# Optimization experiments

Hardware: AMD Instinct MI355X
Metric: run time of the kernel (lower is better)

## Reference

```python
import jax, jax.numpy as jnp
import numpy as np

T, B, OBS, H, P, L, A = 512, 128, 512, 256, 128, 4, 4


def _ln(x, scale, bias, eps=1e-6):
    mu = jnp.mean(x, axis=-1, keepdims=True)
    var = jnp.mean((x - mu) ** 2, axis=-1, keepdims=True)
    return (x - mu) * jax.lax.rsqrt(var + eps) * scale + bias


def _binop(qi, qj):
    # S5 reset-aware associative operator: elements (A, b, reset_flag)
    Ai, bi, ci = qi
    Aj, bj, cj = qj
    A = (Aj * Ai) * (1.0 - cj) + Aj * cj
    b = (Aj * bi + bj) * (1.0 - cj) + bj * cj
    c = ci * (1.0 - cj) + cj
    return A, b, c


def _s5_layer(x, dones, h0, scale, bias, lam_re, lam_im, b_re, b_im, c_re, c_im, d_vec, log_step, glu_W, glu_b):
    # x: (T,B,H) real, dones: (T,B), h0: (B,P) complex64
    skip = x
    u = _ln(x, scale, bias)                                  # prenorm
    lam = lam_re + 1j * lam_im                               # (P,)
    step = jnp.exp(log_step)                                 # (P,)
    lam_bar = jnp.exp(lam * step)                            # ZOH discretization
    B_bar = ((lam_bar - 1.0) / lam)[:, None] * (b_re + 1j * b_im)  # (P,H)
    Bu = jnp.einsum('tbh,ph->tbp', u.astype(jnp.complex64), B_bar)  # (T,B,P)
    A_el = jnp.concatenate([jnp.ones((1, B, P), jnp.complex64),
                            jnp.broadcast_to(lam_bar.astype(jnp.complex64), (T, B, P))], axis=0)
    b_el = jnp.concatenate([h0[None], Bu], axis=0)
    c_el = jnp.concatenate([jnp.zeros((1, B, 1), jnp.float32), dones[..., None]], axis=0)
    _, xs, _ = jax.lax.associative_scan(_binop, (A_el, b_el, c_el), axis=0)
    xs = xs[1:]                                              # (T,B,P) complex states
    new_h = xs[-1]
    C = c_re + 1j * c_im                                     # (H,P)
    ys = 2.0 * jnp.real(jnp.einsum('tbp,hp->tbh', xs, C)) + d_vec * u  # conj_sym output + D*u
    z = _ln(ys, scale, bias)                                 # gtrxl norm (shared LayerNorm params)
    z = jax.nn.gelu(z)                                       # half_glu1
    z = z * jax.nn.sigmoid(z @ glu_W + glu_b)
    return skip + z, new_h


def setup_inputs() -> dict:
    key = jax.random.key(0)
    ks = jax.random.split(key, 40)
    f32 = jnp.float32

    def n(i, shape, s=1.0):
        return jax.random.normal(ks[i], shape, f32) * s

    inp = {}
    inp['obs'] = n(0, (T, B, OBS))
    inp['dones'] = (jax.random.uniform(ks[1], (T, B)) < 0.01).astype(f32)
    inp['hidden_re'] = jnp.zeros((L, B, P), f32)
    inp['hidden_im'] = jnp.zeros((L, B, P), f32)
    inp['enc0_W'] = n(2, (OBS, 128), 1.0 / np.sqrt(OBS))
    inp['enc0_b'] = jnp.zeros((128,), f32)
    inp['enc1_W'] = n(3, (128, H), 1.0 / np.sqrt(128))
    inp['enc1_b'] = jnp.zeros((H,), f32)
    inp['norm_scale'] = jnp.ones((L, H), f32)
    inp['norm_bias'] = jnp.zeros((L, H), f32)
    inp['Lambda_re'] = -0.5 * jax.random.uniform(ks[4], (L, P), f32) - 0.1
    inp['Lambda_im'] = n(5, (L, P), np.pi)
    inp['B_re'] = n(6, (L, P, H), 1.0 / np.sqrt(H))
    inp['B_im'] = n(7, (L, P, H), 1.0 / np.sqrt(H))
    inp['C_re'] = n(8, (L, H, P), 1.0 / np.sqrt(2 * P))
    inp['C_im'] = n(9, (L, H, P), 1.0 / np.sqrt(2 * P))
    inp['D'] = n(10, (L, H))
    inp['log_step'] = jax.random.uniform(ks[11], (L, P), f32, np.log(1e-3), np.log(1e-1))
    inp['glu_W'] = n(12, (L, H, H), 1.0 / np.sqrt(H))
    inp['glu_b'] = jnp.zeros((L, H), f32)
    inp['ab0_W'] = n(13, (H, 128), 1.0 / np.sqrt(H))
    inp['ab0_b'] = jnp.zeros((128,), f32)
    inp['ab1_W'] = n(14, (128, 128), 1.0 / np.sqrt(128))
    inp['ab1_b'] = jnp.zeros((128,), f32)
    inp['adec_W'] = n(15, (128, A), 0.01 / np.sqrt(128))
    inp['adec_b'] = jnp.full((A,), 0.5, f32)
    inp['log_std'] = jnp.full((A,), -0.7, f32)
    inp['vb0_W'] = n(16, (H, 128), 1.0 / np.sqrt(H))
    inp['vb0_b'] = jnp.zeros((128,), f32)
    inp['vb1_W'] = n(17, (128, 128), 1.0 / np.sqrt(128))
    inp['vb1_b'] = jnp.zeros((128,), f32)
    inp['vdec_W'] = n(18, (128, 1), 1.0 / np.sqrt(128))
    inp['vdec_b'] = jnp.zeros((1,), f32)
    return inp


def reference(obs, dones, hidden_re, hidden_im, enc0_W, enc0_b, enc1_W, enc1_b,
              norm_scale, norm_bias, Lambda_re, Lambda_im, B_re, B_im, C_re, C_im,
              D, log_step, glu_W, glu_b, ab0_W, ab0_b, ab1_W, ab1_b, adec_W, adec_b,
              log_std, vb0_W, vb0_b, vb1_W, vb1_b, vdec_W, vdec_b):
    e = jax.nn.leaky_relu(obs @ enc0_W + enc0_b)
    e = jax.nn.leaky_relu(e @ enc1_W + enc1_b)
    h0 = (hidden_re + 1j * hidden_im).astype(jnp.complex64)  # (L,B,P)
    new_h = []
    for l in range(L):
        e, hl = _s5_layer(e, dones, h0[l], norm_scale[l], norm_bias[l],
                          Lambda_re[l], Lambda_im[l], B_re[l], B_im[l],
                          C_re[l], C_im[l], D[l], log_step[l], glu_W[l], glu_b[l])
        new_h.append(hl)
    new_h = jnp.stack(new_h)
    am = jax.nn.leaky_relu(e @ ab0_W + ab0_b)
    am = jax.nn.leaky_relu(am @ ab1_W + ab1_b)
    am = am @ adec_W + adec_b                                # actor mean (T,B,A)
    v = jax.nn.leaky_relu(e @ vb0_W + vb0_b)
    v = jax.nn.leaky_relu(v @ vb1_W + vb1_b)
    v = v @ vdec_W + vdec_b                                  # critic (T,B,1)
    sc = jnp.broadcast_to(jnp.exp(log_std), am.shape)        # Normal scale (pi params)
    out = jnp.concatenate([am, sc, v], axis=-1)              # (T,B,2A+1)
    return out, jnp.real(new_h), jnp.imag(new_h)
```

## Files before the change

kernel.cpp:

```cpp
#include <hip/hip_runtime.h>
#include <math.h>

#define TT 512
#define BB 128
#define OBSD 512
#define HD 256
#define PD 128
#define LD 4
#define NTB (TT*BB)

typedef __bf16 bf16x8 __attribute__((ext_vector_type(8)));
typedef float  f32x4  __attribute__((ext_vector_type(4)));

__device__ __forceinline__ float bf2f(unsigned short u) {
    return __uint_as_float(((unsigned)u) << 16);
}
__device__ __forceinline__ unsigned short f2bf(float f) {
    unsigned u = __float_as_uint(f);
    unsigned r = (u + 0x7FFFu + ((u >> 16) & 1u)) >> 16;
    return (unsigned short)r;
}
__device__ __forceinline__ float gelu_f(float x) {
    float x3 = x * x * x;
    return 0.5f * x * (1.f + tanhf(0.7978845608028654f * (x + 0.044715f * x3)));
}

template<int MODE, int NJ>
__global__ __launch_bounds__(256) void mgemm2(
    const unsigned short* __restrict__ A, const unsigned short* __restrict__ BT,
    int K, const float* __restrict__ bias,
    const float* __restrict__ lnsc, const float* __restrict__ lnbi,
    const unsigned short* __restrict__ aux1, unsigned short* Xio,
    unsigned short* __restrict__ U, int wU)
{
    const int N = NJ * 64;
    __shared__ unsigned short smA[64 * 32];
    __shared__ unsigned short smB[NJ * 64 * 32];
    __shared__ float2 red[64][4];
    int tid = threadIdx.x;
    int lane = tid & 63, w = tid >> 6;
    int m16 = lane & 15, quad = lane >> 4;
    int m0 = blockIdx.x * 64;

    f32x4 acc[4][NJ] = {};

    for (int k0 = 0; k0 < K; k0 += 32) {
        {
            const unsigned short* g = A + (size_t)(m0 + (tid >> 2)) * K + k0 + (tid & 3) * 8;
            unsigned short* l = smA + tid * 8;
            __builtin_amdgcn_global_load_lds(
                (const __attribute__((address_space(1))) void*)g,
                (__attribute__((address_space(3))) void*)l, 16, 0, 0);
        }
#pragma unroll
        for (int p = 0; p < NJ; ++p) {
            const unsigned short* g = BT + (size_t)(p * 64 + (tid >> 2)) * K + k0 + (tid & 3) * 8;
            unsigned short* l = smB + p * 2048 + tid * 8;
            __builtin_amdgcn_global_load_lds(
                (const __attribute__((address_space(1))) void*)g,
                (__attribute__((address_space(3))) void*)l, 16, 0, 0);
        }
        __syncthreads();
        bf16x8 af[4], bfr[NJ];
#pragma unroll
        for (int mi = 0; mi < 4; ++mi)
            af[mi] = *(const bf16x8*)(smA + (mi * 16 + m16) * 32 + quad * 8);
#pragma unroll
        for (int nj = 0; nj < NJ; ++nj)
            bfr[nj] = *(const bf16x8*)(smB + (w * NJ * 16 + nj * 16 + m16) * 32 + quad * 8);
#pragma unroll
        for (int mi = 0; mi < 4; ++mi)
#pragma unroll
            for (int nj = 0; nj < NJ; ++nj)
                acc[mi][nj] = __builtin_amdgcn_mfma_f32_16x16x32_bf16(
                    bfr[nj], af[mi], acc[mi][nj], 0, 0, 0);
        __syncthreads();
    }

    int colb = w * NJ * 16 + quad * 4;

    if (MODE == 1) {
#pragma unroll
        for (int mi = 0; mi < 4; ++mi) {
            size_t rowb = (size_t)(m0 + mi * 16 + m16) * N;
#pragma unroll
            for (int nj = 0; nj < NJ; ++nj) {
                ushort4 o = { f2bf(acc[mi][nj][0]), f2bf(acc[mi][nj][1]),
                              f2bf(acc[mi][nj][2]), f2bf(acc[mi][nj][3]) };
                *(ushort4*)(U + rowb + colb + nj * 16) = o;
            }
        }
        return;
    }

    float4 bn[NJ];
#pragma unroll
    for (int nj = 0; nj < NJ; ++nj) bn[nj] = *(const float4*)(bias + colb + nj * 16);

#pragma unroll
    for (int mi = 0; mi < 4; ++mi) {
        size_t rowb = (size_t)(m0 + mi * 16 + m16) * N;
        float s = 0.f, q = 0.f;
#pragma unroll
        for (int nj = 0; nj < NJ; ++nj) {
            ushort4 a1, xo;
            if (MODE == 2 || MODE == 3) a1 = *(const ushort4*)(aux1 + rowb + colb + nj * 16);
            if (MODE == 3)              xo = *(const ushort4*)(Xio + rowb + colb + nj * 16);
            float vv[4];
#pragma unroll
            for (int r = 0; r < 4; ++r) {
                float v = acc[mi][nj][r];
                float bv = (r == 0) ? bn[nj].x : (r == 1) ? bn[nj].y : (r == 2) ? bn[nj].z : bn[nj].w;
                if (MODE == 0 || MODE == 4) {
                    v += bv; v = v > 0.f ? v : 0.01f * v;
                } else if (MODE == 2) {
                    float u = bf2f(r == 0 ? a1.x : r == 1 ? a1.y : r == 2 ? a1.z : a1.w);
                    v += bv * u;
                } else if (MODE == 3) {
                    float zz = bf2f(r == 0 ? a1.x : r == 1 ? a1.y : r == 2 ? a1.z : a1.w);
                    float xx = bf2f(r == 0 ? xo.x : r == 1 ? xo.y : r == 2 ? xo.z : xo.w);
                    float sg = 1.f / (1.f + expf(-(v + bv)));
                    v = xx + zz * sg;
                }
                vv[r] = v;
                acc[mi][nj][r] = v;
                s += v; q += v * v;
            }
            if (MODE == 0 || MODE == 3) {
                ushort4 o = { f2bf(vv[0]), f2bf(vv[1]), f2bf(vv[2]), f2bf(vv[3]) };
                *(ushort4*)(Xio + rowb + colb + nj * 16) = o;
            } else if (MODE == 4) {
                ushort4 o = { f2bf(vv[0]), f2bf(vv[1]), f2bf(vv[2]), f2bf(vv[3]) };
                *(ushort4*)(U + rowb + colb + nj * 16) = o;
            }
        }
        if (MODE != 4 && (MODE != 3 || wU)) {
            s += __shfl_xor(s, 16); q += __shfl_xor(q, 16);
            s += __shfl_xor(s, 32); q += __shfl_xor(q, 32);
            if (quad == 0) red[mi * 16 + m16][w] = float2{s, q};
        }
    }
    if (MODE == 4 || (MODE == 3 && !wU)) return;
    __syncthreads();

    float4 ls[NJ], lb[NJ];
#pragma unroll
    for (int nj = 0; nj < NJ; ++nj) {
        ls[nj] = *(const float4*)(lnsc + colb + nj * 16);
        lb[nj] = *(const float4*)(lnbi + colb + nj * 16);
    }
#pragma unroll
    for (int mi = 0; mi < 4; ++mi) {
        int row_l = mi * 16 + m16;
        float2 t0 = red[row_l][0], t1 = red[row_l][1], t2 = red[row_l][2], t3 = red[row_l][3];
        float S = t0.x + t1.x + t2.x + t3.x;
        float Q = t0.y + t1.y + t2.y + t3.y;
        float mu = S * (1.f / 256.f);
        float var = Q * (1.f / 256.f) - mu * mu;
        float rstd = rsqrtf(var + 1e-6f);
        size_t rowb = (size_t)(m0 + row_l) * N;
#pragma unroll
        for (int nj = 0; nj < NJ; ++nj) {
            float o[4];
#pragma unroll
            for (int r = 0; r < 4; ++r) {
                float sc = (r == 0) ? ls[nj].x : (r == 1) ? ls[nj].y : (r == 2) ? ls[nj].z : ls[nj].w;
                float bi = (r == 0) ? lb[nj].x : (r == 1) ? lb[nj].y : (r == 2) ? lb[nj].z : lb[nj].w;
                float v = (acc[mi][nj][r] - mu) * rstd * sc + bi;
                if (MODE == 2) v = gelu_f(v);
                o[r] = v;
            }
            ushort4 ov = { f2bf(o[0]), f2bf(o[1]), f2bf(o[2]), f2bf(o[3]) };
            *(ushort4*)(U + rowb + colb + nj * 16) = ov;
        }
    }
}

__global__ __launch_bounds__(256) void mgemm_obs(
    const float* __restrict__ A, const unsigned short* __restrict__ BT,
    unsigned short* __restrict__ U, const float* __restrict__ bias)
{
    const int K = 512, NJ = 2, N = 128;
    __shared__ unsigned short smA[64 * 32];
    __shared__ unsigned short smB[NJ * 64 * 32];
    int tid = threadIdx.x;
    int lane = tid & 63, w = tid >> 6;
    int m16 = lane & 15, quad = lane >> 4;
    int m0 = blockIdx.x * 64;

    f32x4 acc[4][NJ] = {};
    for (int k0 = 0; k0 < K; k0 += 32) {
#pragma unroll
        for (int p = 0; p < 2; ++p) {
            int idx = p * 256 + tid;
            int r = idx >> 3, kq = (idx & 7) * 4;
            float4 v = *(const float4*)(A + (size_t)(m0 + r) * K + k0 + kq);
            ushort4 o = { f2bf(v.x), f2bf(v.y), f2bf(v.z), f2bf(v.w) };
            *(ushort4*)(smA + r * 32 + kq) = o;
        }
#pragma unroll
        for (int p = 0; p < NJ; ++p) {
            const unsigned short* g = BT + (size_t)(p * 64 + (tid >> 2)) * K + k0 + (tid & 3) * 8;
            unsigned short* l = smB + p * 2048 + tid * 8;
            __builtin_amdgcn_global_load_lds(
                (const __attribute__((address_space(1))) void*)g,
                (__attribute__((address_space(3))) void*)l, 16, 0, 0);
        }
        __syncthreads();
        bf16x8 af[4], bfr[NJ];
#pragma unroll
        for (int mi = 0; mi < 4; ++mi)
            af[mi] = *(const bf16x8*)(smA + (mi * 16 + m16) * 32 + quad * 8);
#pragma unroll
        for (int nj = 0; nj < NJ; ++nj)
            bfr[nj] = *(const bf16x8*)(smB + (w * NJ * 16 + nj * 16 + m16) * 32 + quad * 8);
#pragma unroll
        for (int mi = 0; mi < 4; ++mi)
#pragma unroll
            for (int nj = 0; nj < NJ; ++nj)
                acc[mi][nj] = __builtin_amdgcn_mfma_f32_16x16x32_bf16(
                    bfr[nj], af[mi], acc[mi][nj], 0, 0, 0);
        __syncthreads();
    }
    int colb = w * NJ * 16 + quad * 4;
#pragma unroll
    for (int mi = 0; mi < 4; ++mi) {
        size_t rowb = (size_t)(m0 + mi * 16 + m16) * N;
#pragma unroll
        for (int nj = 0; nj < NJ; ++nj) {
            float4 bv = *(const float4*)(bias + colb + nj * 16);
            float v0 = acc[mi][nj][0] + bv.x; v0 = v0 > 0.f ? v0 : 0.01f * v0;
            float v1 = acc[mi][nj][1] + bv.y; v1 = v1 > 0.f ? v1 : 0.01f * v1;
            float v2 = acc[mi][nj][2] + bv.z; v2 = v2 > 0.f ? v2 : 0.01f * v2;
            float v3 = acc[mi][nj][3] + bv.w; v3 = v3 > 0.f ? v3 : 0.01f * v3;
            ushort4 o = { f2bf(v0), f2bf(v1), f2bf(v2), f2bf(v3) };
            *(ushort4*)(U + rowb + colb + nj * 16) = o;
        }
    }
}

__global__ __launch_bounds__(512) void scan2_k(
    const unsigned short* __restrict__ bu, unsigned short* __restrict__ xs,
    const float* __restrict__ dones,
    const float* __restrict__ h0re, const float* __restrict__ h0im,
    const float* __restrict__ lamre, const float* __restrict__ lamim,
    const float* __restrict__ lstep,
    float* __restrict__ outre, float* __restrict__ outim)
{
    __shared__ float sdone[TT];
    __shared__ float4 ssum[8][64];
    __shared__ float2 shin[8][64];
    int tid = threadIdx.x;
    int b  = blockIdx.x >> 1;
    int ph = blockIdx.x & 1;
    int chunk = tid >> 6, pl = tid & 63;
    int p = ph * 64 + pl;
    sdone[tid] = dones[tid * BB + b];
    float lr = lamre[p], li = lamim[p];
    float st = expf(lstep[p]);
    float er = expf(lr * st);
    float ar = er * cosf(li * st);
    float ai = er * sinf(li * st);
    __syncthreads();

    int t0 = chunk * 64;
    unsigned buf[64];
    float Ar = 1.f, Ai = 0.f, br = 0.f, bi = 0.f;
#pragma unroll
    for (int j = 0; j < 64; ++j) {
        size_t off = ((size_t)(t0 + j) * BB + b) * 256 + 2 * p;
        unsigned v = *(const unsigned*)(bu + off);
        buf[j] = v;
        float bur = bf2f((unsigned short)(v & 0xFFFFu));
        float bui = bf2f((unsigned short)(v >> 16));
        if (sdone[t0 + j] != 0.f) {
            Ar = 0.f; Ai = 0.f; br = bur; bi = bui;
        } else {
            float nAr = ar * Ar - ai * Ai;
            float nAi = ar * Ai + ai * Ar;
            float nbr = fmaf(ar, br, fmaf(-ai, bi, bur));
            float nbi = fmaf(ar, bi, fmaf(ai, br, bui));
            Ar = nAr; Ai = nAi; br = nbr; bi = nbi;
        }
    }
    ssum[chunk][pl] = float4{Ar, Ai, br, bi};
    __syncthreads();
    if (tid < 64) {
        int gid = b * 128 + p;
        float hr = h0re[gid], hi = h0im[gid];
#pragma unroll
        for (int c = 0; c < 8; ++c) {
            shin[c][pl] = float2{hr, hi};
            float4 s = ssum[c][pl];
            float nhr = fmaf(s.x, hr, fmaf(-s.y, hi, s.z));
            float nhi = fmaf(s.x, hi, fmaf(s.y, hr, s.w));
            hr = nhr; hi = nhi;
        }
        outre[gid] = hr; outim[gid] = hi;
    }
    __syncthreads();
    float hr = shin[chunk][pl].x, hi = shin[chunk][pl].y;
#pragma unroll
    for (int j = 0; j < 64; ++j) {
        unsigned v = buf[j];
        float bur = bf2f((unsigned short)(v & 0xFFFFu));
        float bui = bf2f((unsigned short)(v >> 16));
        float nr, ni;
        if (sdone[t0 + j] != 0.f) { nr = bur; ni = bui; }
        else {
            nr = fmaf(ar, hr, fmaf(-ai, hi, bur));
            ni = fmaf(ar, hi, fmaf(ai, hr, bui));
        }
        hr = nr; hi = ni;
        size_t off = ((size_t)(t0 + j) * BB + b) * 256 + 2 * p;
        *(unsigned*)(xs + off) = ((unsigned)f2bf(ni) << 16) | f2bf(nr);
    }
}

__global__ __launch_bounds__(256) void prep_k(
    const float* __restrict__ Br, const float* __restrict__ Bi,
    const float* __restrict__ Cr, const float* __restrict__ Ci,
    const float* __restrict__ Lr, const float* __restrict__ Li,
    const float* __restrict__ ls, unsigned short* bbarT, unsigned short* ccatT)
{
    int gid = blockIdx.x * 256 + threadIdx.x;
    int l = gid >> 15;
    int rem = gid & 32767;
    int p = rem >> 8;
    int h = rem & 255;
    float lr = Lr[l * PD + p], li = Li[l * PD + p];
    float st = expf(ls[l * PD + p]);
    float er = expf(lr * st);
    float lbr = er * cosf(li * st);
    float lbi = er * sinf(li * st);
    float nr = lbr - 1.f, ni = lbi;
    float den = lr * lr + li * li;
    float fr = (nr * lr + ni * li) / den;
    float fi = (ni * lr - nr * li) / den;
    float bre = Br[(size_t)(l * PD + p) * HD + h];
    float bim = Bi[(size_t)(l * PD + p) * HD + h];
    size_t lb = (size_t)l * 65536;
    bbarT[lb + (size_t)(2 * p) * 256 + h]     = f2bf(fr * bre - fi * bim);
    bbarT[lb + (size_t)(2 * p + 1) * 256 + h] = f2bf(fr * bim + fi * bre);
    float cre = Cr[(size_t)(l * HD + h) * PD + p];
    float cim = Ci[(size_t)(l * HD + h) * PD + p];
    ccatT[lb + (size_t)h * 256 + 2 * p]     = f2bf(2.f * cre);
    ccatT[lb + (size_t)h * 256 + 2 * p + 1] = f2bf(-2.f * cim);
}

__global__ __launch_bounds__(256) void tcvt_k(const float* __restrict__ in,
    unsigned short* __restrict__ out, int K, int N)
{
    int gid = blockIdx.x * 256 + threadIdx.x;
    if (gid >= K * N) return;
    int k = gid / N, n = gid - k * N;
    out[(size_t)n * K + k] = f2bf(in[gid]);
}

__global__ __launch_bounds__(256) void head_k(
    const unsigned short* __restrict__ am2, const unsigned short* __restrict__ v2,
    const float* __restrict__ adW, const float* __restrict__ adb,
    const float* __restrict__ lstd,
    const float* __restrict__ vdW, const float* __restrict__ vdb,
    float* out)
{
    int wid = threadIdx.x >> 6, lane = threadIdx.x & 63;
    size_t row = (size_t)blockIdx.x * 4 + wid;
    float a1 = bf2f(am2[row * 128 + lane]);
    float a2 = bf2f(am2[row * 128 + 64 + lane]);
    float w1 = bf2f(v2[row * 128 + lane]);
    float w2 = bf2f(v2[row * 128 + 64 + lane]);
    float vals[5];
#pragma unroll
    for (int a = 0; a < 4; ++a)
        vals[a] = a1 * adW[lane * 4 + a] + a2 * adW[(lane + 64) * 4 + a];
    vals[4] = w1 * vdW[lane] + w2 * vdW[64 + lane];
#pragma unroll
    for (int off = 32; off; off >>= 1)
#pragma unroll
        for (int k = 0; k < 5; ++k) vals[k] += __shfl_xor(vals[k], off);
    if (lane == 0) {
        size_t o = row * 9;
#pragma unroll
        for (int a = 0; a < 4; ++a) out[o + a] = vals[a] + adb[a];
#pragma unroll
        for (int a = 0; a < 4; ++a) out[o + 4 + a] = expf(lstd[a]);
        out[o + 8] = vals[4] + vdb[0];
    }
}

extern "C" void kernel_launch(void* const* d_in, const int* in_sizes, int n_in,
                              void* d_out, int out_size, void* d_ws, size_t ws_size,
                              hipStream_t stream) {
    (void)in_sizes; (void)n_in; (void)out_size; (void)ws_size;
    const float* obs     = (const float*)d_in[0];
    const float* dones   = (const float*)d_in[1];
    const float* hre     = (const float*)d_in[2];
    const float* him     = (const float*)d_in[3];
    const float* enc0_W  = (const float*)d_in[4];
    const float* enc0_b  = (const float*)d_in[5];
    const float* enc1_W  = (const float*)d_in[6];
    const float* enc1_b  = (const float*)d_in[7];
    const float* nsc     = (const float*)d_in[8];
    const float* nbi     = (const float*)d_in[9];
    const float* Lre     = (const float*)d_in[10];
    const float* Lim     = (const float*)d_in[11];
    const float* B_re    = (const float*)d_in[12];
    const float* B_im    = (const float*)d_in[13];
    const float* C_re    = (const float*)d_in[14];
    const float* C_im    = (const float*)d_in[15];
    const float* Dv      = (const float*)d_in[16];
    const float* lstep   = (const float*)d_in[17];
    const float* glu_W   = (const float*)d_in[18];
    const float* glu_b   = (const float*)d_in[19];
    const float* ab0_W   = (const float*)d_in[20];
    const float* ab0_b   = (const float*)d_in[21];
    const float* ab1_W   = (const float*)d_in[22];
    const float* ab1_b   = (const float*)d_in[23];
    const float* adec_W  = (const float*)d_in[24];
    const float* adec_b  = (const float*)d_in[25];
    const float* log_std = (const float*)d_in[26];
    const float* vb0_W   = (const float*)d_in[27];
    const float* vb0_b   = (const float*)d_in[28];
    const float* vb1_W   = (const float*)d_in[29];
    const float* vb1_b   = (const float*)d_in[30];
    const float* vdec_W  = (const float*)d_in[31];
    const float* vdec_b  = (const float*)d_in[32];

    const size_t MB = (size_t)1 << 20;
    char* wsb = (char*)d_ws;
    unsigned short* XS    = (unsigned short*)(wsb);
    unsigned short* AM1   = (unsigned short*)(wsb);
    unsigned short* V1    = (unsigned short*)(wsb + 16 * MB);
    unsigned short* AM2   = (unsigned short*)(wsb + 32 * MB);
    unsigned short* V2    = (unsigned short*)(wsb + 48 * MB);
    unsigned short* U1    = (unsigned short*)(wsb + 64 * MB);
    unsigned short* X     = (unsigned short*)(wsb + 96 * MB);
    unsigned short* U     = (unsigned short*)(wsb + 128 * MB);
    unsigned short* BU    = (unsigned short*)(wsb + 160 * MB);
    char* wgt = wsb + 192 * MB;
    unsigned short* BBART = (unsigned short*)(wgt);
    unsigned short* CCATT = (unsigned short*)(wgt + 512 * 1024);
    unsigned short* GLUT  = (unsigned short*)(wgt + 1024 * 1024);
    unsigned short* E0T   = (unsigned short*)(wgt + 1536 * 1024);
    unsigned short* E1T   = (unsigned short*)(wgt + 1664 * 1024);
    unsigned short* AB0T  = (unsigned short*)(wgt + 1728 * 1024);
    unsigned short* AB1T  = (unsigned short*)(wgt + 1792 * 1024);
    unsigned short* VB0T  = (unsigned short*)(wgt + 1824 * 1024);
    unsigned short* VB1T  = (unsigned short*)(wgt + 1888 * 1024);

    float* out   = (float*)d_out;
    float* outre = out + (size_t)NTB * 9;
    float* outim = outre + LD * BB * PD;

    prep_k<<<512, 256, 0, stream>>>(B_re, B_im, C_re, C_im, Lre, Lim, lstep, BBART, CCATT);
    tcvt_k<<<256, 256, 0, stream>>>(enc0_W, E0T, 512, 128);
    tcvt_k<<<128, 256, 0, stream>>>(enc1_W, E1T, 128, 256);
    for (int l = 0; l < LD; ++l)
        tcvt_k<<<256, 256, 0, stream>>>(glu_W + (size_t)l * 65536, GLUT + (size_t)l * 65536, 256, 256);
    tcvt_k<<<128, 256, 0, stream>>>(ab0_W, AB0T, 256, 128);
    tcvt_k<<<64, 256, 0, stream>>>(ab1_W, AB1T, 128, 128);
    tcvt_k<<<128, 256, 0, stream>>>(vb0_W, VB0T, 256, 128);
    tcvt_k<<<64, 256, 0, stream>>>(vb1_W, VB1T, 128, 128);

    mgemm_obs<<<1024, 256, 0, stream>>>(obs, E0T, U1, enc0_b);
    mgemm2<0, 4><<<1024, 256, 0, stream>>>(U1, E1T, 128, enc1_b, nsc, nbi, nullptr, X, U, 1);

    for (int l = 0; l < LD; ++l) {
        mgemm2<1, 4><<<1024, 256, 0, stream>>>(U, BBART + (size_t)l * 65536, 256,
                                               nullptr, nullptr, nullptr, nullptr, nullptr, BU, 0);
        scan2_k<<<256, 512, 0, stream>>>(BU, XS, dones, hre + l * BB * PD, him + l * BB * PD,
                                         Lre + l * PD, Lim + l * PD, lstep + l * PD,
                                         outre + l * BB * PD, outim + l * BB * PD);
        mgemm2<2, 4><<<1024, 256, 0, stream>>>(XS, CCATT + (size_t)l * 65536, 256,
                                               Dv + l * HD, nsc + l * HD, nbi + l * HD, U, nullptr, U, 1);
        const float* nsc2 = nsc + ((l + 1 < LD) ? (l + 1) * HD : 0);
        const float* nbi2 = nbi + ((l + 1 < LD) ? (l + 1) * HD : 0);
        mgemm2<3, 4><<<1024, 256, 0, stream>>>(U, GLUT + (size_t)l * 65536, 256,
                                               glu_b + l * HD, nsc2, nbi2, U, X, U, (l + 1 < LD) ? 1 : 0);
    }

    mgemm2<4, 2><<<1024, 256, 0, stream>>>(X, AB0T, 256, ab0_b, nullptr, nullptr, nullptr, nullptr, AM1, 0);
    mgemm2<4, 2><<<1024, 256, 0, stream>>>(AM1, AB1T, 128, ab1_b, nullptr, nullptr, nullptr, nullptr, AM2, 0);
    mgemm2<4, 2><<<1024, 256, 0, stream>>>(X, VB0T, 256, vb0_b, nullptr, nullptr, nullptr, nullptr, V1, 0);
    mgemm2<4, 2><<<1024, 256, 0, stream>>>(V1, VB1T, 128, vb1_b, nullptr, nullptr, nullptr, nullptr, V2, 0);
    head_k<<<NTB / 4, 256, 0, stream>>>(AM2, V2, adec_W, adec_b, log_std, vdec_W, vdec_b, out);
}
```

Baseline: 984.7 us.

## Fuse chained per-layer GEMMs through LDS-resident intermediates and merge head MLPs

Replaces the separate C-projection, GLU and next-layer B-projection GEMM launches with one fused kernel per layer. Each block keeps its 64-row normalized activation tile in shared memory and feeds it straight into the next GEMM. This avoids writing and re-reading the U intermediate through global memory and cuts the number of launches. The actor and critic head MLPs plus the decoder are fused into a single two-way grid kernel, and the weight transposes are merged into one launch. The cost is much larger shared-memory use per block (about 34KB for the z buffer plus a larger B tile), which may lower occupancy.

```diff
diff --git a/kernel.cpp b/kernel.cpp
--- a/kernel.cpp
+++ b/kernel.cpp
@@ -24,130 +24,115 @@
     float x3 = x * x * x;
     return 0.5f * x * (1.f + tanhf(0.7978845608028654f * (x + 0.044715f * x3)));
 }
-
-template<int MODE, int NJ>
-__global__ __launch_bounds__(256) void mgemm2(
-    const unsigned short* __restrict__ A, const unsigned short* __restrict__ BT,
-    int K, const float* __restrict__ bias,
-    const float* __restrict__ lnsc, const float* __restrict__ lnbi,
-    const unsigned short* __restrict__ aux1, unsigned short* Xio,
-    unsigned short* __restrict__ U, int wU)
-{
-    const int N = NJ * 64;
+__device__ __forceinline__ float lane4(float4 v, int r) {
+    return (r == 0) ? v.x : (r == 1) ? v.y : (r == 2) ? v.z : v.w;
+}
+
+__device__ __forceinline__ void stgA(const unsigned short* A, int ldk, int m0, int k0,
+                                     unsigned short* smA, int tid)
+{
+    const unsigned short* g = A + (size_t)(m0 + (tid >> 2)) * ldk + k0 + (tid & 3) * 8;
+    __builtin_amdgcn_global_load_lds(
+        (const __attribute__((address_space(1))) void*)g,
+        (__attribute__((address_space(3))) void*)(smA + tid * 8), 16, 0, 0);
+}
+template<int NR>
+__device__ __forceinline__ void stgB(const unsigned short* BT, int ldk, int k0,
+                                     unsigned short* smB, int tid)
+{
+#pragma unroll
+    for (int p = 0; p < NR / 64; ++p) {
+        const unsigned short* g = BT + (size_t)(p * 64 + (tid >> 2)) * ldk + k0 + (tid & 3) * 8;
+        __builtin_amdgcn_global_load_lds(
+            (const __attribute__((address_space(1))) void*)g,
+            (__attribute__((address_space(3))) void*)(smB + p * 2048 + tid * 8), 16, 0, 0);
+    }
+}
+
+template<int VAR>
+__global__ __launch_bounds__(256, 2) void fused_k(
+    const unsigned short* __restrict__ A, const unsigned short* __restrict__ BT1, int K1,
+    const float* __restrict__ bias1, const float* __restrict__ ln1s, const float* __restrict__ ln1b,
+    const unsigned short* __restrict__ auxU,
+    const unsigned short* __restrict__ BT2, const float* __restrict__ bias2,
+    const float* __restrict__ ln2s, const float* __restrict__ ln2b,
+    unsigned short* __restrict__ X, unsigned short* __restrict__ Uout,
+    const unsigned short* __restrict__ BT3, unsigned short* __restrict__ BU)
+{
+    const int ZS = 264;
     __shared__ unsigned short smA[64 * 32];
-    __shared__ unsigned short smB[NJ * 64 * 32];
+    __shared__ unsigned short smB[256 * 32];
+    __shared__ unsigned short zbuf[64 * ZS];
     __shared__ float2 red[64][4];
     int tid = threadIdx.x;
     int lane = tid & 63, w = tid >> 6;
     int m16 = lane & 15, quad = lane >> 4;
     int m0 = blockIdx.x * 64;
-
-    f32x4 acc[4][NJ] = {};
-
-    for (int k0 = 0; k0 < K; k0 += 32) {
-        {
-            const unsigned short* g = A + (size_t)(m0 + (tid >> 2)) * K + k0 + (tid & 3) * 8;
-            unsigned short* l = smA + tid * 8;
-            __builtin_amdgcn_global_load_lds(
-                (const __attribute__((address_space(1))) void*)g,
-                (__attribute__((address_space(3))) void*)l, 16, 0, 0);
-        }
-#pragma unroll
-        for (int p = 0; p < NJ; ++p) {
-            const unsigned short* g = BT + (size_t)(p * 64 + (tid >> 2)) * K + k0 + (tid & 3) * 8;
-            unsigned short* l = smB + p * 2048 + tid * 8;
-            __builtin_amdgcn_global_load_lds(
-                (const __attribute__((address_space(1))) void*)g,
-                (__attribute__((address_space(3))) void*)l, 16, 0, 0);
-        }
-        __syncthreads();
-        bf16x8 af[4], bfr[NJ];
+    int colb = w * 64 + quad * 4;
+
+    f32x4 acc[4][4] = {};
+    for (int k0 = 0; k0 < K1; k0 += 32) {
+        stgA(A, K1, m0, k0, smA, tid);
+        stgB<256>(BT1, K1, k0, smB, tid);
+        __syncthreads();
+        bf16x8 af[4], bfr[4];
 #pragma unroll
         for (int mi = 0; mi < 4; ++mi)
             af[mi] = *(const bf16x8*)(smA + (mi * 16 + m16) * 32 + quad * 8);
 #pragma unroll
-        for (int nj = 0; nj < NJ; ++nj)
-            bfr[nj] = *(const bf16x8*)(smB + (w * NJ * 16 + nj * 16 + m16) * 32 + quad * 8);
-#pragma unroll
-        for (int mi = 0; mi < 4; ++mi)
-#pragma unroll
-            for (int nj = 0; nj < NJ; ++nj)
+        for (int nj = 0; nj < 4; ++nj)
+            bfr[nj] = *(const bf16x8*)(smB + (w * 64 + nj * 16 + m16) * 32 + quad * 8);
+#pragma unroll
+        for (int mi = 0; mi < 4; ++mi)
+#pragma unroll
+            for (int nj = 0; nj < 4; ++nj)
                 acc[mi][nj] = __builtin_amdgcn_mfma_f32_16x16x32_bf16(
                     bfr[nj], af[mi], acc[mi][nj], 0, 0, 0);
         __syncthreads();
     }
 
-    int colb = w * NJ * 16 + quad * 4;
-
-    if (MODE == 1) {
-#pragma unroll
-        for (int mi = 0; mi < 4; ++mi) {
-            size_t rowb = (size_t)(m0 + mi * 16 + m16) * N;
-#pragma unroll
-            for (int nj = 0; nj < NJ; ++nj) {
-                ushort4 o = { f2bf(acc[mi][nj][0]), f2bf(acc[mi][nj][1]),
-                              f2bf(acc[mi][nj][2]), f2bf(acc[mi][nj][3]) };
-                *(ushort4*)(U + rowb + colb + nj * 16) = o;
-            }
-        }
-        return;
-    }
-
-    float4 bn[NJ];
-#pragma unroll
-    for (int nj = 0; nj < NJ; ++nj) bn[nj] = *(const float4*)(bias + colb + nj * 16);
-
-#pragma unroll
-    for (int mi = 0; mi < 4; ++mi) {
-        size_t rowb = (size_t)(m0 + mi * 16 + m16) * N;
+    float4 bn[4];
+#pragma unroll
+    for (int nj = 0; nj < 4; ++nj) bn[nj] = *(const float4*)(bias1 + colb + nj * 16);
+
+#pragma unroll
+    for (int mi = 0; mi < 4; ++mi) {
+        size_t rowb = (size_t)(m0 + mi * 16 + m16) * 256;
         float s = 0.f, q = 0.f;
 #pragma unroll
-        for (int nj = 0; nj < NJ; ++nj) {
-            ushort4 a1, xo;
-            if (MODE == 2 || MODE == 3) a1 = *(const ushort4*)(aux1 + rowb + colb + nj * 16);
-            if (MODE == 3)              xo = *(const ushort4*)(Xio + rowb + colb + nj * 16);
+        for (int nj = 0; nj < 4; ++nj) {
+            ushort4 a1;
+            if (VAR != 0) a1 = *(const ushort4*)(auxU + rowb + colb + nj * 16);
             float vv[4];
 #pragma unroll
             for (int r = 0; r < 4; ++r) {
                 float v = acc[mi][nj][r];
-                float bv = (r == 0) ? bn[nj].x : (r == 1) ? bn[nj].y : (r == 2) ? bn[nj].z : bn[nj].w;
-                if (MODE == 0 || MODE == 4) {
+                float bv = lane4(bn[nj], r);
+                if (VAR == 0) {
                     v += bv; v = v > 0.f ? v : 0.01f * v;
-                } else if (MODE == 2) {
-                    float u = bf2f(r == 0 ? a1.x : r == 1 ? a1.y : r == 2 ? a1.z : a1.w);
-                    v += bv * u;
-                } else if (MODE == 3) {
-                    float zz = bf2f(r == 0 ? a1.x : r == 1 ? a1.y : r == 2 ? a1.z : a1.w);
-                    float xx = bf2f(r == 0 ? xo.x : r == 1 ? xo.y : r == 2 ? xo.z : xo.w);
-                    float sg = 1.f / (1.f + expf(-(v + bv)));
-                    v = xx + zz * sg;
+                } else {
+                    float uu = bf2f(r == 0 ? a1.x : r == 1 ? a1.y : r == 2 ? a1.z : a1.w);
+                    v += bv * uu;
                 }
-                vv[r] = v;
-                acc[mi][nj][r] = v;
+                vv[r] = v; acc[mi][nj][r] = v;
                 s += v; q += v * v;
             }
-            if (MODE == 0 || MODE == 3) {
+            if (VAR == 0) {
                 ushort4 o = { f2bf(vv[0]), f2bf(vv[1]), f2bf(vv[2]), f2bf(vv[3]) };
-                *(ushort4*)(Xio + rowb + colb + nj * 16) = o;
-            } else if (MODE == 4) {
-                ushort4 o = { f2bf(vv[0]), f2bf(vv[1]), f2bf(vv[2]), f2bf(vv[3]) };
-                *(ushort4*)(U + rowb + colb + nj * 16) = o;
+                *(ushort4*)(X + rowb + colb + nj * 16) = o;
             }
         }
-        if (MODE != 4 && (MODE != 3 || wU)) {
-            s += __shfl_xor(s, 16); q += __shfl_xor(q, 16);
-            s += __shfl_xor(s, 32); q += __shfl_xor(q, 32);
-            if (quad == 0) red[mi * 16 + m16][w] = float2{s, q};
-        }
-    }
-    if (MODE == 4 || (MODE == 3 && !wU)) return;
-    __syncthreads();
-
-    float4 ls[NJ], lb[NJ];
-#pragma unroll
-    for (int nj = 0; nj < NJ; ++nj) {
-        ls[nj] = *(const float4*)(lnsc + colb + nj * 16);
-        lb[nj] = *(const float4*)(lnbi + colb + nj * 16);
+        s += __shfl_xor(s, 16); q += __shfl_xor(q, 16);
+        s += __shfl_xor(s, 32); q += __shfl_xor(q, 32);
+        if (quad == 0) red[mi * 16 + m16][w] = float2{s, q};
+    }
+    __syncthreads();
+
+    float4 l1s[4], l1b[4];
+#pragma unroll
+    for (int nj = 0; nj < 4; ++nj) {
+        l1s[nj] = *(const float4*)(ln1s + colb + nj * 16);
+        l1b[nj] = *(const float4*)(ln1b + colb + nj * 16);
     }
 #pragma unroll
     for (int mi = 0; mi < 4; ++mi) {
@@ -156,22 +141,273 @@
         float S = t0.x + t1.x + t2.x + t3.x;
         float Q = t0.y + t1.y + t2.y + t3.y;
         float mu = S * (1.f / 256.f);
-        float var = Q * (1.f / 256.f) - mu * mu;
-        float rstd = rsqrtf(var + 1e-6f);
-        size_t rowb = (size_t)(m0 + row_l) * N;
-#pragma unroll
-        for (int nj = 0; nj < NJ; ++nj) {
+        float rstd = rsqrtf(Q * (1.f / 256.f) - mu * mu + 1e-6f);
+        size_t rowb = (size_t)(m0 + row_l) * 256;
+#pragma unroll
+        for (int nj = 0; nj < 4; ++nj) {
             float o[4];
 #pragma unroll
             for (int r = 0; r < 4; ++r) {
-                float sc = (r == 0) ? ls[nj].x : (r == 1) ? ls[nj].y : (r == 2) ? ls[nj].z : ls[nj].w;
-                float bi = (r == 0) ? lb[nj].x : (r == 1) ? lb[nj].y : (r == 2) ? lb[nj].z : lb[nj].w;
-                float v = (acc[mi][nj][r] - mu) * rstd * sc + bi;
-                if (MODE == 2) v = gelu_f(v);
-                o[r] = v;
+                float v = (acc[mi][nj][r] - mu) * rstd * lane4(l1s[nj], r) + lane4(l1b[nj], r);
+                if (VAR != 0) v = gelu_f(v);
+                o[r] = v; acc[mi][nj][r] = v;
             }
             ushort4 ov = { f2bf(o[0]), f2bf(o[1]), f2bf(o[2]), f2bf(o[3]) };
-            *(ushort4*)(U + rowb + colb + nj * 16) = ov;
+            *(ushort4*)(zbuf + row_l * ZS + colb + nj * 16) = ov;
+            if (VAR == 0) *(ushort4*)(Uout + rowb + colb + nj * 16) = ov;
+        }
+    }
+    __syncthreads();
+
+    const unsigned short* Bm2 = (VAR == 0) ? BT3 : BT2;
+    f32x4 acc2[4][4] = {};
+    for (int k0 = 0; k0 < 256; k0 += 32) {
+        stgB<256>(Bm2, 256, k0, smB, tid);
+        __syncthreads();
+        bf16x8 af[4], bfr[4];
+#pragma unroll
+        for (int mi = 0; mi < 4; ++mi)
+            af[mi] = *(const bf16x8*)(zbuf + (mi * 16 + m16) * ZS + k0 + quad * 8);
+#pragma unroll
+        for (int nj = 0; nj < 4; ++nj)
+            bfr[nj] = *(const bf16x8*)(smB + (w * 64 + nj * 16 + m16) * 32 + quad * 8);
+#pragma unroll
+        for (int mi = 0; mi < 4; ++mi)
+#pragma unroll
+            for (int nj = 0; nj < 4; ++nj)
+                acc2[mi][nj] = __builtin_amdgcn_mfma_f32_16x16x32_bf16(
+                    bfr[nj], af[mi], acc2[mi][nj], 0, 0, 0);
+        __syncthreads();
+    }
+
+    if (VAR == 0) {
+#pragma unroll
+        for (int mi = 0; mi < 4; ++mi) {
+            size_t rowb = (size_t)(m0 + mi * 16 + m16) * 256;
+#pragma unroll
+            for (int nj = 0; nj < 4; ++nj) {
+                ushort4 o = { f2bf(acc2[mi][nj][0]), f2bf(acc2[mi][nj][1]),
+                              f2bf(acc2[mi][nj][2]), f2bf(acc2[mi][nj][3]) };
+                *(ushort4*)(BU + rowb + colb + nj * 16) = o;
+            }
+        }
+        return;
+    }
+
+    float4 b2[4];
+#pragma unroll
+    for (int nj = 0; nj < 4; ++nj) b2[nj] = *(const float4*)(bias2 + colb + nj * 16);
+#pragma unroll
+    for (int mi = 0; mi < 4; ++mi) {
+        size_t rowb = (size_t)(m0 + mi * 16 + m16) * 256;
+        float s = 0.f, q = 0.f;
+#pragma unroll
+        for (int nj = 0; nj < 4; ++nj) {
+            ushort4 xo = *(const ushort4*)(X + rowb + colb + nj * 16);
+            float vv[4];
+#pragma unroll
+            for (int r = 0; r < 4; ++r) {
+                float g = acc2[mi][nj][r] + lane4(b2[nj], r);
+                float sg = 1.f / (1.f + expf(-g));
+                float xx = bf2f(r == 0 ? xo.x : r == 1 ? xo.y : r == 2 ? xo.z : xo.w);
+                float v = xx + acc[mi][nj][r] * sg;
+                vv[r] = v; acc2[mi][nj][r] = v;
+                s += v; q += v * v;
+            }
+            ushort4 o = { f2bf(vv[0]), f2bf(vv[1]), f2bf(vv[2]), f2bf(vv[3]) };
+            *(ushort4*)(X + rowb + colb + nj * 16) = o;
+        }
+        if (VAR == 1) {
+            s += __shfl_xor(s, 16); q += __shfl_xor(q, 16);
+            s += __shfl_xor(s, 32); q += __shfl_xor(q, 32);
+            if (quad == 0) red[mi * 16 + m16][w] = float2{s, q};
+        }
+    }
+    if (VAR == 2) return;
+    __syncthreads();
+
+    float4 l2s[4], l2b[4];
+#pragma unroll
+    for (int nj = 0; nj < 4; ++nj) {
+        l2s[nj] = *(const float4*)(ln2s + colb + nj * 16);
+        l2b[nj] = *(const float4*)(ln2b + colb + nj * 16);
+    }
+#pragma unroll
+    for (int mi = 0; mi < 4; ++mi) {
+        int row_l = mi * 16 + m16;
+        float2 t0 = red[row_l][0], t1 = red[row_l][1], t2 = red[row_l][2], t3 = red[row_l][3];
+        float S = t0.x + t1.x + t2.x + t3.x;
+        float Q = t0.y + t1.y + t2.y + t3.y;
+        float mu = S * (1.f / 256.f);
+        float rstd = rsqrtf(Q * (1.f / 256.f) - mu * mu + 1e-6f);
+        size_t rowb = (size_t)(m0 + row_l) * 256;
+#pragma unroll
+        for (int nj = 0; nj < 4; ++nj) {
+            float o[4];
+#pragma unroll
+            for (int r = 0; r < 4; ++r)
+                o[r] = (acc2[mi][nj][r] - mu) * rstd * lane4(l2s[nj], r) + lane4(l2b[nj], r);
+            ushort4 ov = { f2bf(o[0]), f2bf(o[1]), f2bf(o[2]), f2bf(o[3]) };
+            *(ushort4*)(zbuf + row_l * ZS + colb + nj * 16) = ov;
+            *(ushort4*)(Uout + rowb + colb + nj * 16) = ov;
+        }
+    }
+    __syncthreads();
+
+    f32x4 acc3[4][4] = {};
+    for (int k0 = 0; k0 < 256; k0 += 32) {
+        stgB<256>(BT3, 256, k0, smB, tid);
+        __syncthreads();
+        bf16x8 af[4], bfr[4];
+#pragma unroll
+        for (int mi = 0; mi < 4; ++mi)
+            af[mi] = *(const bf16x8*)(zbuf + (mi * 16 + m16) * ZS + k0 + quad * 8);
+#pragma unroll
+        for (int nj = 0; nj < 4; ++nj)
+            bfr[nj] = *(const bf16x8*)(smB + (w * 64 + nj * 16 + m16) * 32 + quad * 8);
+#pragma unroll
+        for (int mi = 0; mi < 4; ++mi)
+#pragma unroll
+            for (int nj = 0; nj < 4; ++nj)
+                acc3[mi][nj] = __builtin_amdgcn_mfma_f32_16x16x32_bf16(
+                    bfr[nj], af[mi], acc3[mi][nj], 0, 0, 0);
+        __syncthreads();
+    }
+#pragma unroll
+    for (int mi = 0; mi < 4; ++mi) {
+        size_t rowb = (size_t)(m0 + mi * 16 + m16) * 256;
+#pragma unroll
+        for (int nj = 0; nj < 4; ++nj) {
+            ushort4 o = { f2bf(acc3[mi][nj][0]), f2bf(acc3[mi][nj][1]),
+                          f2bf(acc3[mi][nj][2]), f2bf(acc3[mi][nj][3]) };
+            *(ushort4*)(BU + rowb + colb + nj * 16) = o;
+        }
+    }
+}
+
+__global__ __launch_bounds__(256) void head2_k(
+    const unsigned short* __restrict__ X,
+    const unsigned short* __restrict__ AB0T, const float* __restrict__ ab0_b,
+    const unsigned short* __restrict__ AB1T, const float* __restrict__ ab1_b,
+    const unsigned short* __restrict__ VB0T, const float* __restrict__ vb0_b,
+    const unsigned short* __restrict__ VB1T, const float* __restrict__ vb1_b,
+    const float* __restrict__ adW, const float* __restrict__ adb,
+    const float* __restrict__ lstd,
+    const float* __restrict__ vdW, const float* __restrict__ vdb,
+    float* __restrict__ out)
+{
+    const int HS = 136;
+    __shared__ unsigned short smA[64 * 32];
+    __shared__ unsigned short smB[128 * 32];
+    __shared__ unsigned short hbuf[64 * HS];
+    __shared__ float4 redh[64][4];
+    int tid = threadIdx.x;
+    int lane = tid & 63, w = tid >> 6;
+    int m16 = lane & 15, quad = lane >> 4;
+    int m0 = blockIdx.x * 64;
+    int y = blockIdx.y;
+    int colb = w * 32 + quad * 4;
+
+    const unsigned short* BT1 = y ? VB0T : AB0T;
+    const unsigned short* BT2 = y ? VB1T : AB1T;
+    const float* b0 = y ? vb0_b : ab0_b;
+    const float* b1 = y ? vb1_b : ab1_b;
+
+    f32x4 acc[4][2] = {};
+    for (int k0 = 0; k0 < 256; k0 += 32) {
+        stgA(X, 256, m0, k0, smA, tid);
+        stgB<128>(BT1, 256, k0, smB, tid);
+        __syncthreads();
+        bf16x8 af[4], bfr[2];
+#pragma unroll
+        for (int mi = 0; mi < 4; ++mi)
+            af[mi] = *(const bf16x8*)(smA + (mi * 16 + m16) * 32 + quad * 8);
+#pragma unroll
+        for (int nj = 0; nj < 2; ++nj)
+            bfr[nj] = *(const bf16x8*)(smB + (w * 32 + nj * 16 + m16) * 32 + quad * 8);
+#pragma unroll
+        for (int mi = 0; mi < 4; ++mi)
+#pragma unroll
+            for (int nj = 0; nj < 2; ++nj)
+                acc[mi][nj] = __builtin_amdgcn_mfma_f32_16x16x32_bf16(
+                    bfr[nj], af[mi], acc[mi][nj], 0, 0, 0);
+        __syncthreads();
+    }
+#pragma unroll
+    for (int mi = 0; mi < 4; ++mi) {
+#pragma unroll
+        for (int nj = 0; nj < 2; ++nj) {
+            float4 bv = *(const float4*)(b0 + colb + nj * 16);
+            float o[4];
+#pragma unroll
+            for (int r = 0; r < 4; ++r) {
+                float v = acc[mi][nj][r] + lane4(bv, r);
+                o[r] = v > 0.f ? v : 0.01f * v;
+            }
+            ushort4 ov = { f2bf(o[0]), f2bf(o[1]), f2bf(o[2]), f2bf(o[3]) };
+            *(ushort4*)(hbuf + (mi * 16 + m16) * HS + colb + nj * 16) = ov;
+        }
+    }
+    __syncthreads();
+
+    f32x4 acc2[4][2] = {};
+    for (int k0 = 0; k0 < 128; k0 += 32) {
+        stgB<128>(BT2, 128, k0, smB, tid);
+        __syncthreads();
+        bf16x8 af[4], bfr[2];
+#pragma unroll
+        for (int mi = 0; mi < 4; ++mi)
+            af[mi] = *(const bf16x8*)(hbuf + (mi * 16 + m16) * HS + k0 + quad * 8);
+#pragma unroll
+        for (int nj = 0; nj < 2; ++nj)
+            bfr[nj] = *(const bf16x8*)(smB + (w * 32 + nj * 16 + m16) * 32 + quad * 8);
+#pragma unroll
+        for (int mi = 0; mi < 4; ++mi)
+#pragma unroll
+            for (int nj = 0; nj < 2; ++nj)
+                acc2[mi][nj] = __builtin_amdgcn_mfma_f32_16x16x32_bf16(
+                    bfr[nj], af[mi], acc2[mi][nj], 0, 0, 0);
+        __syncthreads();
+    }
+#pragma unroll
+    for (int mi = 0; mi < 4; ++mi) {
+        float4 part = {0.f, 0.f, 0.f, 0.f};
+#pragma unroll
+        for (int nj = 0; nj < 2; ++nj) {
+            float4 bv = *(const float4*)(b1 + colb + nj * 16);
+#pragma unroll
+            for (int r = 0; r < 4; ++r) {
+                float v = acc2[mi][nj][r] + lane4(bv, r);
+                v = v > 0.f ? v : 0.01f * v;
+                int c = colb + nj * 16 + r;
+                if (y == 0) {
+                    float4 wv = *(const float4*)(adW + c * 4);
+                    part.x += v * wv.x; part.y += v * wv.y;
+                    part.z += v * wv.z; part.w += v * wv.w;
+                } else {
+                    part.x += v * vdW[c];
+                }
+            }
+        }
+        part.x += __shfl_xor(part.x, 16); part.x += __shfl_xor(part.x, 32);
+        part.y += __shfl_xor(part.y, 16); part.y += __shfl_xor(part.y, 32);
+        part.z += __shfl_xor(part.z, 16); part.z += __shfl_xor(part.z, 32);
+        part.w += __shfl_xor(part.w, 16); part.w += __shfl_xor(part.w, 32);
+        if (quad == 0) redh[mi * 16 + m16][w] = part;
+    }
+    __syncthreads();
+    if (tid < 64) {
+        float4 t0 = redh[tid][0], t1 = redh[tid][1], t2 = redh[tid][2], t3 = redh[tid][3];
+        size_t o = (size_t)(m0 + tid) * 9;
+        if (y == 0) {
+            out[o + 0] = t0.x + t1.x + t2.x + t3.x + adb[0];
+            out[o + 1] = t0.y + t1.y + t2.y + t3.y + adb[1];
+            out[o + 2] = t0.z + t1.z + t2.z + t3.z + adb[2];
+            out[o + 3] = t0.w + t1.w + t2.w + t3.w + adb[3];
+#pragma unroll
+            for (int a = 0; a < 4; ++a) out[o + 4 + a] = expf(lstd[a]);
+        } else {
+            out[o + 8] = t0.x + t1.x + t2.x + t3.x + vdb[0];
         }
     }
 }
@@ -198,14 +434,7 @@
             ushort4 o = { f2bf(v.x), f2bf(v.y), f2bf(v.z), f2bf(v.w) };
             *(ushort4*)(smA + r * 32 + kq) = o;
         }
-#pragma unroll
-        for (int p = 0; p < NJ; ++p) {
-            const unsigned short* g = BT + (size_t)(p * 64 + (tid >> 2)) * K + k0 + (tid & 3) * 8;
-            unsigned short* l = smB + p * 2048 + tid * 8;
-            __builtin_amdgcn_global_load_lds(
-                (const __attribute__((address_space(1))) void*)g,
-                (__attribute__((address_space(3))) void*)l, 16, 0, 0);
-        }
+        stgB<128>(BT, K, k0, smB, tid);
         __syncthreads();
         bf16x8 af[4], bfr[NJ];
 #pragma unroll
@@ -348,45 +577,27 @@
     ccatT[lb + (size_t)h * 256 + 2 * p + 1] = f2bf(-2.f * cim);
 }
 
-__global__ __launch_bounds__(256) void tcvt_k(const float* __restrict__ in,
-    unsigned short* __restrict__ out, int K, int N)
+__global__ __launch_bounds__(256) void tcvt_all(
+    const float* __restrict__ e0, const float* __restrict__ e1,
+    const float* __restrict__ glu, const float* __restrict__ a0,
+    const float* __restrict__ a1, const float* __restrict__ v0,
+    const float* __restrict__ v1,
+    unsigned short* E0T, unsigned short* E1T, unsigned short* GLUT,
+    unsigned short* AB0T, unsigned short* AB1T, unsigned short* VB0T,
+    unsigned short* VB1T)
 {
     int gid = blockIdx.x * 256 + threadIdx.x;
-    if (gid >= K * N) return;
-    int k = gid / N, n = gid - k * N;
-    out[(size_t)n * K + k] = f2bf(in[gid]);
-}
-
-__global__ __launch_bounds__(256) void head_k(
-    const unsigned short* __restrict__ am2, const unsigned short* __restrict__ v2,
-    const float* __restrict__ adW, const float* __restrict__ adb,
-    const float* __restrict__ lstd,
-    const float* __restrict__ vdW, const float* __restrict__ vdb,
-    float* out)
-{
-    int wid = threadIdx.x >> 6, lane = threadIdx.x & 63;
-    size_t row = (size_t)blockIdx.x * 4 + wid;
-    float a1 = bf2f(am2[row * 128 + lane]);
-    float a2 = bf2f(am2[row * 128 + 64 + lane]);
-    float w1 = bf2f(v2[row * 128 + lane]);
-    float w2 = bf2f(v2[row * 128 + 64 + lane]);
-    float vals[5];
-#pragma unroll
-    for (int a = 0; a < 4; ++a)
-        vals[a] = a1 * adW[lane * 4 + a] + a2 * adW[(lane + 64) * 4 + a];
-    vals[4] = w1 * vdW[lane] + w2 * vdW[64 + lane];
-#pragma unroll
-    for (int off = 32; off; off >>= 1)
-#pragma unroll
-        for (int k = 0; k < 5; ++k) vals[k] += __shfl_xor(vals[k], off);
-    if (lane == 0) {
-        size_t o = row * 9;
-#pragma unroll
-        for (int a = 0; a < 4; ++a) out[o + a] = vals[a] + adb[a];
-#pragma unroll
-        for (int a = 0; a < 4; ++a) out[o + 4 + a] = expf(lstd[a]);
-        out[o + 8] = vals[4] + vdb[0];
-    }
+    const float* in; unsigned short* outp; int K, N, local;
+    if (gid < 65536)       { in = e0; outp = E0T; K = 512; N = 128; local = gid; }
+    else if (gid < 98304)  { in = e1; outp = E1T; K = 128; N = 256; local = gid - 65536; }
+    else if (gid < 360448) { local = gid - 98304; int l = local >> 16; local &= 65535;
+                             in = glu + (size_t)l * 65536; outp = GLUT + (size_t)l * 65536; K = 256; N = 256; }
+    else if (gid < 393216) { in = a0; outp = AB0T; K = 256; N = 128; local = gid - 360448; }
+    else if (gid < 409600) { in = a1; outp = AB1T; K = 128; N = 128; local = gid - 393216; }
+    else if (gid < 442368) { in = v0; outp = VB0T; K = 256; N = 128; local = gid - 409600; }
+    else                   { in = v1; outp = VB1T; K = 128; N = 128; local = gid - 442368; }
+    int k = local / N, n = local - k * N;
+    outp[(size_t)n * K + k] = f2bf(in[local]);
 }
 
 extern "C" void kernel_launch(void* const* d_in, const int* in_sizes, int n_in,
@@ -430,10 +641,6 @@
     const size_t MB = (size_t)1 << 20;
     char* wsb = (char*)d_ws;
     unsigned short* XS    = (unsigned short*)(wsb);
-    unsigned short* AM1   = (unsigned short*)(wsb);
-    unsigned short* V1    = (unsigned short*)(wsb + 16 * MB);
-    unsigned short* AM2   = (unsigned short*)(wsb + 32 * MB);
-    unsigned short* V2    = (unsigned short*)(wsb + 48 * MB);
     unsigned short* U1    = (unsigned short*)(wsb + 64 * MB);
     unsigned short* X     = (unsigned short*)(wsb + 96 * MB);
     unsigned short* U     = (unsigned short*)(wsb + 128 * MB);
@@ -454,35 +661,34 @@
     float* outim = outre + LD * BB * PD;
 
     prep_k<<<512, 256, 0, stream>>>(B_re, B_im, C_re, C_im, Lre, Lim, lstep, BBART, CCATT);
-    tcvt_k<<<256, 256, 0, stream>>>(enc0_W, E0T, 512, 128);
-    tcvt_k<<<128, 256, 0, stream>>>(enc1_W, E1T, 128, 256);
-    for (int l = 0; l < LD; ++l)
-        tcvt_k<<<256, 256, 0, stream>>>(glu_W + (size_t)l * 65536, GLUT + (size_t)l * 65536, 256, 256);
-    tcvt_k<<<128, 256, 0, stream>>>(ab0_W, AB0T, 256, 128);
-    tcvt_k<<<64, 256, 0, stream>>>(ab1_W, AB1T, 128, 128);
-    tcvt_k<<<128, 256, 0, stream>>>(vb0_W, VB0T, 256, 128);
-    tcvt_k<<<64, 256, 0, stream>>>(vb1_W, VB1T, 128, 128);
+    tcvt_all<<<1792, 256, 0, stream>>>(enc0_W, enc1_W, glu_W, ab0_W, ab1_W, vb0_W, vb1_W,
+                                       E0T, E1T, GLUT, AB0T, AB1T, VB0T, VB1T);
 
     mgemm_obs<<<1024, 256, 0, stream>>>(obs, E0T, U1, enc0_b);
-    mgemm2<0, 4><<<1024, 256, 0, stream>>>(U1, E1T, 128, enc1_b, nsc, nbi, nullptr, X, U, 1);
+    fused_k<0><<<1024, 256, 0, stream>>>(U1, E1T, 128, enc1_b, nsc, nbi,
+                                         nullptr, nullptr, nullptr, nullptr, nullptr,
+                                         X, U, BBART, BU);
 
     for (int l = 0; l < LD; ++l) {
-        mgemm2<1, 4><<<1024, 256, 0, stream>>>(U, BBART + (size_t)l * 65536, 256,
-                                               nullptr, nullptr, nullptr, nullptr, nullptr, BU, 0);
         scan2_k<<<256, 512, 0, stream>>>(BU, XS, dones, hre + l * BB * PD, him + l * BB * PD,
                                          Lre + l * PD, Lim + l * PD, lstep + l * PD,
                                          outre + l * BB * PD, outim + l * BB * PD);
-        mgemm2<2, 4><<<1024, 256, 0, stream>>>(XS, CCATT + (size_t)l * 65536, 256,
-                                               Dv + l * HD, nsc + l * HD, nbi + l * HD, U, nullptr, U, 1);
-        const float* nsc2 = nsc + ((l + 1 < LD) ? (l + 1) * HD : 0);
-        const float* nbi2 = nbi + ((l + 1 < LD) ? (l + 1) * HD : 0);
-        mgemm2<3, 4><<<1024, 256, 0, stream>>>(U, GLUT + (size_t)l * 65536, 256,
-                                               glu_b + l * HD, nsc2, nbi2, U, X, U, (l + 1 < LD) ? 1 : 0);
-    }
-
-    mgemm2<4, 2><<<1024, 256, 0, stream>>>(X, AB0T, 256, ab0_b, nullptr, nullptr, nullptr, nullptr, AM1, 0);
-    mgemm2<4, 2><<<1024, 256, 0, stream>>>(AM1, AB1T, 128, ab1_b, nullptr, nullptr, nullptr, nullptr, AM2, 0);
-    mgemm2<4, 2><<<1024, 256, 0, stream>>>(X, VB0T, 256, vb0_b, nullptr, nullptr, nullptr, nullptr, V1, 0);
-    mgemm2<4, 2><<<1024, 256, 0, stream>>>(V1, VB1T, 128, vb1_b, nullptr, nullptr, nullptr, nullptr, V2, 0);
-    head_k<<<NTB / 4, 256, 0, stream>>>(AM2, V2, adec_W, adec_b, log_std, vdec_W, vdec_b, out);
-}
+        if (l < LD - 1) {
+            fused_k<1><<<1024, 256, 0, stream>>>(XS, CCATT + (size_t)l * 65536, 256,
+                Dv + l * HD, nsc + l * HD, nbi + l * HD, U,
+                GLUT + (size_t)l * 65536, glu_b + l * HD,
+                nsc + (l + 1) * HD, nbi + (l + 1) * HD,
+                X, U, BBART + (size_t)(l + 1) * 65536, BU);
+        } else {
+            fused_k<2><<<1024, 256, 0, stream>>>(XS, CCATT + (size_t)l * 65536, 256,
+                Dv + l * HD, nsc + l * HD, nbi + l * HD, U,
+                GLUT + (size_t)l * 65536, glu_b + l * HD,
+                nullptr, nullptr,
+                X, nullptr, nullptr, nullptr);
+        }
+    }
+
+    head2_k<<<dim3(1024, 2), 256, 0, stream>>>(X, AB0T, ab0_b, AB1T, ab1_b,
+                                               VB0T, vb0_b, VB1T, vb1_b,
+                                               adec_W, adec_b, log_std, vdec_W, vdec_b, out);
+}
```

New measurement: 1.033 ms. 1.05x slower.
